# Performance work log

Measured on AMD Instinct MI355X. Metric: run time of the kernel, lower is better.

The kernel has to match this reference:

```python
import jax, jax.numpy as jnp
import numpy as np

TH_SIM_MIN = 0.9
TH_DIFF_MAX = 0.1
BIG = 1e9
EPS = 1e-8


def setup_inputs() -> dict:
    key = jax.random.key(0)
    k1, k2 = jax.random.split(key)
    B, T, D = 16, 2048, 128
    embeddings = jax.random.normal(k1, (B, T, D), dtype=jnp.float32)
    label = jax.random.randint(k2, (B, T), 0, 2, dtype=jnp.int32)
    return {"embeddings": embeddings, "label": label}


def _masked_mean(vals, row_mask):
    # mean of vals over rows where row_mask is True; 0-safe denominator
    cnt = jnp.sum(row_mask, axis=-1).astype(vals.dtype)
    s = jnp.sum(jnp.where(row_mask, vals, 0.0), axis=-1)
    return s / jnp.maximum(cnt, 1.0)


def reference(embeddings, label):
    B = embeddings.shape[0]
    # pairwise cosine similarity per batch: [B, T, T]
    w = jnp.linalg.norm(embeddings, axis=-1, keepdims=True)  # [B,T,1]
    sim = jnp.einsum('bid,bjd->bij', embeddings, embeddings)
    sim = sim / jnp.maximum(w * jnp.swapaxes(w, 1, 2), EPS)

    fake = (label == 0)  # [B,T]
    real = (label == 1)
    fake_col = fake[:, None, :]
    real_col = real[:, None, :]

    # f2f: for each fake i, min over fake j (diagonal included, as in torch)
    f2f_min = jnp.min(jnp.where(fake_col, sim, BIG), axis=2)
    loss_f2f = _masked_mean(jnp.maximum(TH_SIM_MIN - f2f_min, 0.0), fake)

    # r2r: for each real i, min over real j
    r2r_min = jnp.min(jnp.where(real_col, sim, BIG), axis=2)
    loss_r2r = _masked_mean(jnp.maximum(TH_SIM_MIN - r2r_min, 0.0), real)

    # f2r: for each fake i, max over real j
    f2r_max = jnp.max(jnp.where(real_col, sim, -BIG), axis=2)
    loss_f2r = _masked_mean(jnp.maximum(f2r_max - TH_DIFF_MAX, 0.0), fake)

    # r2f: for each real i, max over fake j
    r2f_max = jnp.max(jnp.where(fake_col, sim, -BIG), axis=2)
    loss_r2f = _masked_mean(jnp.maximum(r2f_max - TH_DIFF_MAX, 0.0), real)

    # torch code `continue`s (adds nothing) when either class is empty
    valid = (jnp.sum(fake, axis=1) > 0) & (jnp.sum(real, axis=1) > 0)
    per_batch = jnp.where(valid, loss_f2f + loss_r2r + loss_f2r + loss_r2f, 0.0)
    return jnp.sum(per_batch) / B
```

## Files before the change

kernel.cpp:

```cpp
#include <hip/hip_runtime.h>
#include <hip/hip_bf16.h>

typedef __bf16 bf16x8 __attribute__((ext_vector_type(8)));
typedef float  f32x4  __attribute__((ext_vector_type(4)));

namespace {
constexpr int kB = 16;
constexpr int kT = 2048;
constexpr int kD = 128;
constexpr int RB = 64;
constexpr int CT = 64;
constexpr float TH_SIM  = 0.9f;
constexpr float TH_DIFF = 0.1f;
constexpr float BIGF    = 1e9f;
}

static __device__ __forceinline__ void gload_lds16(const short* g, short* l) {
    __builtin_amdgcn_global_load_lds(
        (const __attribute__((address_space(1))) void*)g,
        (__attribute__((address_space(3))) void*)l, 16, 0, 0);
}

__global__ __launch_bounds__(256) void scan_kernel(const int* __restrict__ label,
                                                   int* __restrict__ perm,
                                                   int* __restrict__ cFarr) {
    const int b = blockIdx.x, tid = threadIdx.x;
    const int* lb = label + b * kT;
    int loc[8], cnt = 0;
    #pragma unroll
    for (int j = 0; j < 8; ++j) { loc[j] = (lb[tid * 8 + j] == 0); cnt += loc[j]; }
    __shared__ int s[256];
    s[tid] = cnt;
    __syncthreads();
    for (int off = 1; off < 256; off <<= 1) {
        const int v = (tid >= off) ? s[tid - off] : 0;
        __syncthreads();
        s[tid] += v;
        __syncthreads();
    }
    const int total = s[255];
    if (tid == 0) cFarr[b] = total;
    int run = s[tid] - cnt;
    #pragma unroll
    for (int j = 0; j < 8; ++j) {
        const int i = tid * 8 + j;
        perm[b * kT + i] = loc[j] ? run : (total + i - run);
        run += loc[j];
    }
}

__global__ __launch_bounds__(256) void nrm_kernel(const float* __restrict__ emb,
                                                  const int* __restrict__ perm,
                                                  __hip_bfloat16* __restrict__ out) {
    const int wave = threadIdx.x >> 6;
    const int lane = threadIdx.x & 63;
    const int row  = blockIdx.x * 4 + wave;
    const float2 v = *reinterpret_cast<const float2*>(emb + (size_t)row * kD + lane * 2);
    float ss = v.x * v.x + v.y * v.y;
    #pragma unroll
    for (int m = 1; m < 64; m <<= 1) ss += __shfl_xor(ss, m);
    const float inv = ss > 0.f ? rsqrtf(ss) : 0.f;
    const int b   = row >> 11;
    const int dst = perm[row];
    __hip_bfloat162 o;
    o.x = __float2bfloat16(v.x * inv);
    o.y = __float2bfloat16(v.y * inv);
    *reinterpret_cast<__hip_bfloat162*>(out + ((size_t)(b * kT + dst)) * kD + lane * 2) = o;
}

template <int MODE>
__device__ __forceinline__ void compute_tile(const short* __restrict__ buf,
                                             const bf16x8 (&afrag)[4],
                                             const float (&sgn)[4],
                                             float (&u1)[4], float (&u2)[4],
                                             int lo, int hi, int colBase, int cf) {
    #pragma unroll
    for (int g = 0; g < 4; ++g) {
        const int col = g * 16 + lo;
        bf16x8 bfrag[4];
        #pragma unroll
        for (int kk = 0; kk < 4; ++kk) {
            const int sh = (kk * 32 + hi * 8) ^ ((col & 7) << 3);
            bfrag[kk] = *reinterpret_cast<const bf16x8*>(&buf[col * kD + sh]);
        }
        f32x4 acc = {0.f, 0.f, 0.f, 0.f};
        #pragma unroll
        for (int kk = 0; kk < 4; ++kk)
            acc = __builtin_amdgcn_mfma_f32_16x16x32_bf16(afrag[kk], bfrag[kk], acc, 0, 0, 0);
        if (MODE == 0) {
            #pragma unroll
            for (int r = 0; r < 4; ++r) u1[r] = fminf(u1[r], acc[r] * sgn[r]);
        } else if (MODE == 1) {
            #pragma unroll
            for (int r = 0; r < 4; ++r) u2[r] = fminf(u2[r], -(acc[r] * sgn[r]));
        } else {
            const bool cfake = (colBase + col) < cf;
            #pragma unroll
            for (int r = 0; r < 4; ++r) {
                const float t = acc[r] * sgn[r];
                u1[r] = fminf(u1[r], cfake ? t : BIGF);
                u2[r] = fminf(u2[r], cfake ? BIGF : -t);
            }
        }
    }
}

__global__ __launch_bounds__(256, 2) void crloss_main(const __hip_bfloat16* __restrict__ nrm,
                                                      const int* __restrict__ cFarr,
                                                      float* __restrict__ partials) {
    __shared__ __align__(16) short lds[2][CT * kD];
    const int bid  = blockIdx.x;
    const int b    = bid >> 5;
    const int rb   = bid & 31;
    const int tid  = threadIdx.x;
    const int wave = tid >> 6;
    const int lane = tid & 63;
    const int lo   = lane & 15;
    const int hi   = lane >> 4;

    const short* nb = reinterpret_cast<const short*>(nrm) + (size_t)b * kT * kD;
    const int cf = cFarr[b];
    const int wave_row0 = rb * RB + wave * 16;

    bf16x8 afrag[4];
    #pragma unroll
    for (int kk = 0; kk < 4; ++kk)
        afrag[kk] = *reinterpret_cast<const bf16x8*>(
            nb + (size_t)(wave_row0 + lo) * kD + kk * 32 + hi * 8);

    float sgn[4];
    #pragma unroll
    for (int r = 0; r < 4; ++r)
        sgn[r] = (wave_row0 + hi * 4 + r < cf) ? 1.f : -1.f;

    float u1[4], u2[4];
    #pragma unroll
    for (int r = 0; r < 4; ++r) { u1[r] = BIGF; u2[r] = BIGF; }

    auto stage = [&](int ct, int bufIdx) {
        #pragma unroll
        for (int p = 0; p < 4; ++p) {
            const int unit = p * 4 + wave;
            const int c    = unit * 64 + lane;
            const int col  = c >> 4;
            const int sh   = ((c & 15) * 8) ^ ((col & 7) << 3);
            gload_lds16(nb + (size_t)(ct * CT + col) * kD + sh,
                        &lds[bufIdx][unit * 512]);
        }
    };

    const int  ctF    = cf >> 6;
    const bool hasMix = (cf & 63) != 0;

    stage(0, 0);
    __syncthreads();
    int cur = 0;
    for (int ct = 0; ct < kT / CT; ++ct) {
        if (ct + 1 < kT / CT) stage(ct + 1, cur ^ 1);
        if (ct < ctF)
            compute_tile<0>(lds[cur], afrag, sgn, u1, u2, lo, hi, ct * CT, cf);
        else if (ct == ctF && hasMix)
            compute_tile<2>(lds[cur], afrag, sgn, u1, u2, lo, hi, ct * CT, cf);
        else
            compute_tile<1>(lds[cur], afrag, sgn, u1, u2, lo, hi, ct * CT, cf);
        __syncthreads();
        cur ^= 1;
    }

    #pragma unroll
    for (int m = 1; m <= 8; m <<= 1) {
        #pragma unroll
        for (int r = 0; r < 4; ++r) {
            u1[r] = fminf(u1[r], __shfl_xor(u1[r], m));
            u2[r] = fminf(u2[r], __shfl_xor(u2[r], m));
        }
    }

    float sF = 0.f, sR = 0.f;
    if (lo == 0) {
        #pragma unroll
        for (int r = 0; r < 4; ++r) {
            const int  row = wave_row0 + hi * 4 + r;
            const bool f   = row < cf;
            const float mn = f ? u1[r] : u2[r];
            const float mx = f ? -u2[r] : -u1[r];
            const float l  = fmaxf(TH_SIM - mn, 0.f) + fmaxf(mx - TH_DIFF, 0.f);
            if (f) sF += l; else sR += l;
        }
    }
    #pragma unroll
    for (int m = 1; m < 64; m <<= 1) {
        sF += __shfl_xor(sF, m);
        sR += __shfl_xor(sR, m);
    }

    __shared__ float wsum[4][2];
    if (lane == 0) { wsum[wave][0] = sF; wsum[wave][1] = sR; }
    __syncthreads();
    if (tid == 0) {
        float a = 0.f, c = 0.f;
        for (int w = 0; w < 4; ++w) { a += wsum[w][0]; c += wsum[w][1]; }
        partials[bid * 2]     = a;
        partials[bid * 2 + 1] = c;
    }
}

__global__ __launch_bounds__(512) void crloss_final(const float* __restrict__ partials,
                                                    const int* __restrict__ cFarr,
                                                    float* __restrict__ out) {
    const int t = threadIdx.x;
    float pf = partials[t * 2];
    float pr = partials[t * 2 + 1];
    #pragma unroll
    for (int m = 1; m <= 16; m <<= 1) {
        pf += __shfl_xor(pf, m);
        pr += __shfl_xor(pr, m);
    }
    __shared__ float sF[16], sR[16];
    if ((t & 31) == 0) { sF[t >> 5] = pf; sR[t >> 5] = pr; }
    __syncthreads();
    if (t == 0) {
        float tot = 0.f;
        for (int b = 0; b < kB; ++b) {
            const int cf = cFarr[b], cr = kT - cf;
            if (cf > 0 && cr > 0)
                tot += sF[b] / (float)cf + sR[b] / (float)cr;
        }
        out[0] = tot / (float)kB;
    }
}

extern "C" void kernel_launch(void* const* d_in, const int* in_sizes, int n_in,
                              void* d_out, int out_size, void* d_ws, size_t ws_size,
                              hipStream_t stream) {
    const float* emb   = (const float*)d_in[0];
    const int*   label = (const int*)d_in[1];
    float*       out   = (float*)d_out;

    char* ws = (char*)d_ws;
    __hip_bfloat16* nrm = (__hip_bfloat16*)ws;
    int*   perm     = (int*)(ws + (size_t)kB * kT * kD * 2);
    int*   cFarr    = (int*)(ws + (size_t)kB * kT * kD * 2 + kB * kT * 4);
    float* partials = (float*)(ws + (size_t)kB * kT * kD * 2 + kB * kT * 4 + 64);

    scan_kernel<<<kB, 256, 0, stream>>>(label, perm, cFarr);
    nrm_kernel<<<kB * kT / 4, 256, 0, stream>>>(emb, perm, nrm);
    crloss_main<<<kB * (kT / RB), 256, 0, stream>>>(nrm, cFarr, partials);
    crloss_final<<<1, 512, 0, stream>>>(partials, cFarr, out);
}
```

Measured before the change: 50.86 us.

## Swap wave ownership to all rows times a column slice and fold row signs

Each wave now keeps A fragments for all 64 rows of the block and processes only its own 16 columns of each staged tile. Before, each wave held 16 rows and read all 64 columns, so every wave loaded the whole tile's B fragments from LDS; now each wave loads only a quarter of them. The per-row sign is folded into the A fragments by flipping bf16 sign bits once, which removes the multiply per accumulator element. The cost is a final cross-wave min merge through shared memory, plus more registers for 16 A fragments and 4x more running min/max accumulators per thread.

```diff
diff --git a/kernel.cpp b/kernel.cpp
--- a/kernel.cpp
+++ b/kernel.cpp
@@ -10,6 +10,7 @@
 constexpr int kD = 128;
 constexpr int RB = 64;
 constexpr int CT = 64;
+constexpr int NT = kT / CT;
 constexpr float TH_SIM  = 0.9f;
 constexpr float TH_DIFF = 0.1f;
 constexpr float BIGF    = 1e9f;
@@ -70,36 +71,33 @@
 
 template <int MODE>
 __device__ __forceinline__ void compute_tile(const short* __restrict__ buf,
-                                             const bf16x8 (&afrag)[4],
-                                             const float (&sgn)[4],
-                                             float (&u1)[4], float (&u2)[4],
-                                             int lo, int hi, int colBase, int cf) {
-    #pragma unroll
-    for (int g = 0; g < 4; ++g) {
-        const int col = g * 16 + lo;
-        bf16x8 bfrag[4];
-        #pragma unroll
-        for (int kk = 0; kk < 4; ++kk) {
-            const int sh = (kk * 32 + hi * 8) ^ ((col & 7) << 3);
-            bfrag[kk] = *reinterpret_cast<const bf16x8*>(&buf[col * kD + sh]);
-        }
+                                             const bf16x8 (&afrag)[4][4],
+                                             float (&u1)[4][4], float (&u2)[4][4],
+                                             int col, int hi, int cGlob, int cf) {
+    bf16x8 bfrag[4];
+    #pragma unroll
+    for (int kk = 0; kk < 4; ++kk) {
+        const int sh = (kk * 32 + hi * 8) ^ ((col & 7) << 3);
+        bfrag[kk] = *reinterpret_cast<const bf16x8*>(&buf[col * kD + sh]);
+    }
+    const bool cfake = (MODE == 2) && (cGlob < cf);
+    #pragma unroll
+    for (int rg = 0; rg < 4; ++rg) {
         f32x4 acc = {0.f, 0.f, 0.f, 0.f};
         #pragma unroll
         for (int kk = 0; kk < 4; ++kk)
-            acc = __builtin_amdgcn_mfma_f32_16x16x32_bf16(afrag[kk], bfrag[kk], acc, 0, 0, 0);
+            acc = __builtin_amdgcn_mfma_f32_16x16x32_bf16(afrag[rg][kk], bfrag[kk], acc, 0, 0, 0);
         if (MODE == 0) {
             #pragma unroll
-            for (int r = 0; r < 4; ++r) u1[r] = fminf(u1[r], acc[r] * sgn[r]);
+            for (int r = 0; r < 4; ++r) u1[rg][r] = fminf(u1[rg][r], acc[r]);
         } else if (MODE == 1) {
             #pragma unroll
-            for (int r = 0; r < 4; ++r) u2[r] = fminf(u2[r], -(acc[r] * sgn[r]));
+            for (int r = 0; r < 4; ++r) u2[rg][r] = fminf(u2[rg][r], -acc[r]);
         } else {
-            const bool cfake = (colBase + col) < cf;
             #pragma unroll
             for (int r = 0; r < 4; ++r) {
-                const float t = acc[r] * sgn[r];
-                u1[r] = fminf(u1[r], cfake ? t : BIGF);
-                u2[r] = fminf(u2[r], cfake ? BIGF : -t);
+                u1[rg][r] = fminf(u1[rg][r], cfake ? acc[r] : BIGF);
+                u2[rg][r] = fminf(u2[rg][r], cfake ? BIGF : -acc[r]);
             }
         }
     }
@@ -109,6 +107,7 @@
                                                       const int* __restrict__ cFarr,
                                                       float* __restrict__ partials) {
     __shared__ __align__(16) short lds[2][CT * kD];
+    __shared__ float mrg[2][4][RB];
     const int bid  = blockIdx.x;
     const int b    = bid >> 5;
     const int rb   = bid & 31;
@@ -119,32 +118,38 @@
     const int hi   = lane >> 4;
 
     const short* nb = reinterpret_cast<const short*>(nrm) + (size_t)b * kT * kD;
-    const int cf = cFarr[b];
-    const int wave_row0 = rb * RB + wave * 16;
-
-    bf16x8 afrag[4];
-    #pragma unroll
-    for (int kk = 0; kk < 4; ++kk)
-        afrag[kk] = *reinterpret_cast<const bf16x8*>(
-            nb + (size_t)(wave_row0 + lo) * kD + kk * 32 + hi * 8);
-
-    float sgn[4];
-    #pragma unroll
-    for (int r = 0; r < 4; ++r)
-        sgn[r] = (wave_row0 + hi * 4 + r < cf) ? 1.f : -1.f;
-
-    float u1[4], u2[4];
-    #pragma unroll
-    for (int r = 0; r < 4; ++r) { u1[r] = BIGF; u2[r] = BIGF; }
+    const int cf   = cFarr[b];
+    const int row0 = rb * RB;
+    const int col  = wave * 16 + lo;
+
+    bf16x8 afrag[4][4];
+    #pragma unroll
+    for (int rg = 0; rg < 4; ++rg) {
+        #pragma unroll
+        for (int kk = 0; kk < 4; ++kk)
+            afrag[rg][kk] = *reinterpret_cast<const bf16x8*>(
+                nb + (size_t)(row0 + rg * 16 + lo) * kD + kk * 32 + hi * 8);
+        if (row0 + rg * 16 + lo >= cf) {
+            unsigned* u = reinterpret_cast<unsigned*>(&afrag[rg][0]);
+            #pragma unroll
+            for (int q = 0; q < 16; ++q) u[q] ^= 0x80008000u;
+        }
+    }
+
+    float u1[4][4], u2[4][4];
+    #pragma unroll
+    for (int rg = 0; rg < 4; ++rg)
+        #pragma unroll
+        for (int r = 0; r < 4; ++r) { u1[rg][r] = BIGF; u2[rg][r] = BIGF; }
 
     auto stage = [&](int ct, int bufIdx) {
         #pragma unroll
         for (int p = 0; p < 4; ++p) {
             const int unit = p * 4 + wave;
             const int c    = unit * 64 + lane;
-            const int col  = c >> 4;
-            const int sh   = ((c & 15) * 8) ^ ((col & 7) << 3);
-            gload_lds16(nb + (size_t)(ct * CT + col) * kD + sh,
+            const int scol = c >> 4;
+            const int sh   = ((c & 15) * 8) ^ ((scol & 7) << 3);
+            gload_lds16(nb + (size_t)(ct * CT + scol) * kD + sh,
                         &lds[bufIdx][unit * 512]);
         }
     };
@@ -155,14 +160,14 @@
     stage(0, 0);
     __syncthreads();
     int cur = 0;
-    for (int ct = 0; ct < kT / CT; ++ct) {
-        if (ct + 1 < kT / CT) stage(ct + 1, cur ^ 1);
+    for (int ct = 0; ct < NT; ++ct) {
+        if (ct + 1 < NT) stage(ct + 1, cur ^ 1);
         if (ct < ctF)
-            compute_tile<0>(lds[cur], afrag, sgn, u1, u2, lo, hi, ct * CT, cf);
+            compute_tile<0>(lds[cur], afrag, u1, u2, col, hi, ct * CT + col, cf);
         else if (ct == ctF && hasMix)
-            compute_tile<2>(lds[cur], afrag, sgn, u1, u2, lo, hi, ct * CT, cf);
+            compute_tile<2>(lds[cur], afrag, u1, u2, col, hi, ct * CT + col, cf);
         else
-            compute_tile<1>(lds[cur], afrag, sgn, u1, u2, lo, hi, ct * CT, cf);
+            compute_tile<1>(lds[cur], afrag, u1, u2, col, hi, ct * CT + col, cf);
         __syncthreads();
         cur ^= 1;
     }
@@ -170,38 +175,47 @@
     #pragma unroll
     for (int m = 1; m <= 8; m <<= 1) {
         #pragma unroll
-        for (int r = 0; r < 4; ++r) {
-            u1[r] = fminf(u1[r], __shfl_xor(u1[r], m));
-            u2[r] = fminf(u2[r], __shfl_xor(u2[r], m));
-        }
-    }
-
-    float sF = 0.f, sR = 0.f;
+        for (int rg = 0; rg < 4; ++rg)
+            #pragma unroll
+            for (int r = 0; r < 4; ++r) {
+                u1[rg][r] = fminf(u1[rg][r], __shfl_xor(u1[rg][r], m));
+                u2[rg][r] = fminf(u2[rg][r], __shfl_xor(u2[rg][r], m));
+            }
+    }
+
     if (lo == 0) {
         #pragma unroll
-        for (int r = 0; r < 4; ++r) {
-            const int  row = wave_row0 + hi * 4 + r;
-            const bool f   = row < cf;
-            const float mn = f ? u1[r] : u2[r];
-            const float mx = f ? -u2[r] : -u1[r];
-            const float l  = fmaxf(TH_SIM - mn, 0.f) + fmaxf(mx - TH_DIFF, 0.f);
-            if (f) sF += l; else sR += l;
-        }
-    }
-    #pragma unroll
-    for (int m = 1; m < 64; m <<= 1) {
-        sF += __shfl_xor(sF, m);
-        sR += __shfl_xor(sR, m);
-    }
-
-    __shared__ float wsum[4][2];
-    if (lane == 0) { wsum[wave][0] = sF; wsum[wave][1] = sR; }
-    __syncthreads();
-    if (tid == 0) {
-        float a = 0.f, c = 0.f;
-        for (int w = 0; w < 4; ++w) { a += wsum[w][0]; c += wsum[w][1]; }
-        partials[bid * 2]     = a;
-        partials[bid * 2 + 1] = c;
+        for (int rg = 0; rg < 4; ++rg)
+            #pragma unroll
+            for (int r = 0; r < 4; ++r) {
+                mrg[0][wave][rg * 16 + hi * 4 + r] = u1[rg][r];
+                mrg[1][wave][rg * 16 + hi * 4 + r] = u2[rg][r];
+            }
+    }
+    __syncthreads();
+    if (tid < RB) {
+        const int row = tid;
+        float a1 = BIGF, a2 = BIGF;
+        #pragma unroll
+        for (int w = 0; w < 4; ++w) {
+            a1 = fminf(a1, mrg[0][w][row]);
+            a2 = fminf(a2, mrg[1][w][row]);
+        }
+        const bool f   = (row0 + row) < cf;
+        const float mn = f ? a1 : a2;
+        const float mx = f ? -a2 : -a1;
+        const float l  = fmaxf(TH_SIM - mn, 0.f) + fmaxf(mx - TH_DIFF, 0.f);
+        float sF = f ? l : 0.f;
+        float sR = f ? 0.f : l;
+        #pragma unroll
+        for (int m = 1; m < 64; m <<= 1) {
+            sF += __shfl_xor(sF, m);
+            sR += __shfl_xor(sR, m);
+        }
+        if (tid == 0) {
+            partials[bid * 2]     = sF;
+            partials[bid * 2 + 1] = sR;
+        }
     }
 }
 
```

After: 56.55 us. 1.11x slower.
